# Performance work log

Hardware: AMD Instinct MI355X
Metric: run time of the kernel (lower is better)

## Reference

```python
import jax, jax.numpy as jnp
import numpy as np

B, L, C = 8, 512, 6        # graphs per batch, nodes per graph, atom channels
N = B * L
BOS = 0                    # global-node token id
ATOM_POS_PAD = 0           # atom position pad idx
BIGINT = 1e10

def setup_inputs() -> dict:
    key = jax.random.key(0)
    k1, k2, k3, k4 = jax.random.split(key, 4)
    X = jax.random.normal(k1, (N, C, 3), dtype=jnp.float32) * 5.0
    AP = jax.random.randint(k2, (N, C), 0, 8)              # 0 == atom_pos pad
    S = jax.random.randint(k3, (N,), 1, 16)
    S = S.at[jnp.arange(B) * L].set(BOS)                    # first node of each graph is BOS/global
    sec_pos = jax.random.randint(k4, (N,), 0, 4)
    batch_id = jnp.repeat(jnp.arange(B), L)
    return {"X": X, "AP": AP, "S": S, "sec_pos": sec_pos, "batch_id": batch_id, "k": 9}

def _knn_dist(X, AP, S):
    # per-graph pairwise node distance = min over atom-channel pairs of ||x_ic - x_jd||
    Xb = X.reshape(B, L, C, 3)
    sq = jnp.sum(Xb * Xb, axis=-1)                               # [B,L,C]
    dots = jnp.einsum('bicx,bjdx->bijcd', Xb, Xb)                # [B,L,L,C,C]
    d2 = sq[:, :, None, :, None] + sq[:, None, :, None, :] - 2.0 * dots
    dist = jnp.sqrt(jnp.maximum(d2, 0.0))
    pad = (AP.reshape(B, L, C) == ATOM_POS_PAD)
    pair_pad = pad[:, :, None, :, None] | pad[:, None, :, None, :]
    dist = dist + pair_pad.astype(dist.dtype) * BIGINT
    dist = jnp.min(dist.reshape(B, L, L, C * C), axis=-1)       # [B,L,L]
    # kNN only over non-global (not BOS) endpoints
    glb = (S.reshape(B, L) == BOS)
    gmask = glb[:, :, None] | glb[:, None, :]
    return jnp.where(gmask, jnp.asarray(BIGINT, dist.dtype), dist)

def reference(X, AP, S, sec_pos, batch_id, k):
    dist = _knn_dist(X, AP, S)
    neg_d, dst_local = jax.lax.top_k(-dist, k)                   # smallest-k per row, [B,L,k]
    dknn = (-neg_d).reshape(N, k)
    offs = jnp.arange(B) * L                                      # per-graph node offsets
    dst = (dst_local + offs[:, None, None]).reshape(N, k)
    src = jnp.broadcast_to(jnp.arange(N)[:, None], (N, k))
    valid = dknn < BIGINT
    valid = valid & (sec_pos[src] == sec_pos[dst])               # sec_pos[row]==sec_pos[col] filter
    dst = jnp.where(valid, dst, -1)                              # invalid edges marked -1 (static shape)
    # global edges: (0,j) for all j plus (i,0) for i>=1, per graph
    g_src_l = jnp.concatenate([jnp.zeros(L, jnp.int32), jnp.arange(1, L)])
    g_dst_l = jnp.concatenate([jnp.arange(L), jnp.zeros(L - 1, jnp.int32)])
    glb_edges = jnp.stack([
        (g_src_l[None, :] + offs[:, None]).reshape(-1),
        (g_dst_l[None, :] + offs[:, None]).reshape(-1)])
    # sequential edges among non-global nodes: |i-j|==1, i,j>=1
    a = jnp.arange(1, L - 1)
    s_src_l = jnp.concatenate([a, a + 1])
    s_dst_l = jnp.concatenate([a + 1, a])
    seq_edges = jnp.stack([
        (s_src_l[None, :] + offs[:, None]).reshape(-1),
        (s_dst_l[None, :] + offs[:, None]).reshape(-1)])
    return dknn, src, dst, valid, glb_edges, seq_edges
```

## Files before the change

### kernel.cpp

```cpp
#include <hip/hip_runtime.h>

#define B_  8
#define L_  512
#define C_  6
#define N_  (B_ * L_)
#define K_  9
#define BIGF 1e10f

#define NK        (N_ * K_)
#define OFF_DKNN  0
#define OFF_SRC   (NK)
#define OFF_DST   (2 * NK)
#define OFF_VALID (3 * NK)
#define OFF_GLB   (4 * NK)
#define GLB_PER   (2 * L_ - 1)
#define GLB_TOT   (2 * B_ * GLB_PER)
#define OFF_SEQ   (OFF_GLB + GLB_TOT)
#define SEQ_PER   (2 * (L_ - 2))
#define SEQ_TOT   (2 * B_ * SEQ_PER)

#define TPB 512
#define RPB 8

#define XFLOATS (L_ * C_ * 3)
#define X4      (XFLOATS / 4)
#define AP4     (L_ * C_ / 4)

static __device__ __forceinline__ unsigned umin32(unsigned a, unsigned b) {
    return a < b ? a : b;
}

__global__ __launch_bounds__(TPB, 4) void fused_kernel(const float* __restrict__ X,
                                                       const int* __restrict__ AP,
                                                       const int* __restrict__ S,
                                                       const int* __restrict__ sec,
                                                       float* __restrict__ out) {
    __shared__ float4 ch[C_][L_];
    __shared__ int sbuf[L_];

    const int tid = threadIdx.x;
    const int lane = tid & 63;
    const int wv = tid >> 6;
    const int row = blockIdx.x * RPB + wv;
    const int base = row & ~(L_ - 1);
    const int rl = row & (L_ - 1);

    float* lds = (float*)&ch[0][0];

    {
        const float4* Xs = (const float4*)(X + (size_t)base * (C_ * 3));
        float4* L4 = (float4*)lds;
#pragma unroll
        for (int i = 0; i < 5; ++i) {
            const int idx = tid + i * TPB;
            if (idx < X4) L4[idx] = Xs[idx];
        }
        const int4* As = (const int4*)(AP + (size_t)base * C_);
        int4* LA = (int4*)(lds + XFLOATS);
#pragma unroll
        for (int i = 0; i < 2; ++i) {
            const int idx = tid + i * TPB;
            if (idx < AP4) LA[idx] = As[idx];
        }
        sbuf[tid] = S[base + tid];
    }

    {
        const int gt = blockIdx.x * TPB + tid;
        if (gt < GLB_TOT) {
            const int r = gt / (B_ * GLB_PER);
            const int rem = gt % (B_ * GLB_PER);
            const int b = rem / GLB_PER;
            const int q = rem % GLB_PER;
            int v;
            if (r == 0) v = (q < L_) ? 0 : (q - (L_ - 1));
            else        v = (q < L_) ? q : 0;
            out[OFF_GLB + gt] = (float)(v + b * L_);
        }
        if (gt < SEQ_TOT) {
            const int r = gt / (B_ * SEQ_PER);
            const int rem = gt % (B_ * SEQ_PER);
            const int b = rem / SEQ_PER;
            const int q = rem % SEQ_PER;
            int v;
            if (r == 0) v = (q < L_ - 2) ? (q + 1) : (q - (L_ - 2) + 2);
            else        v = (q < L_ - 2) ? (q + 2) : (q - (L_ - 2) + 1);
            out[OFF_SEQ + gt] = (float)(v + b * L_);
        }
    }

    __syncthreads();

    float4 rrec[C_];
    {
        float xr[18];
        const float2* me = (const float2*)(lds + tid * 18);
#pragma unroll
        for (int j = 0; j < 9; ++j) {
            const float2 t = me[j];
            xr[2 * j] = t.x; xr[2 * j + 1] = t.y;
        }
        const int* apme = ((const int*)(lds + XFLOATS)) + tid * C_;
        int apv[C_];
#pragma unroll
        for (int c = 0; c < C_; ++c) apv[c] = apme[c];
        const float bias_g = (sbuf[tid] == 0) ? BIGF : 0.0f;
#pragma unroll
        for (int c = 0; c < C_; ++c) {
            const float a = xr[3 * c], b = xr[3 * c + 1], d = xr[3 * c + 2];
            float sq = (a * a + b * b) + d * d + bias_g;
            if (apv[c] == 0) sq += BIGF;
            rrec[c] = make_float4(a, b, d, sq);
        }
    }
    __syncthreads();

#pragma unroll
    for (int c = 0; c < C_; ++c) ch[c][tid] = rrec[c];
    __syncthreads();

    float ax[C_], ay[C_], az[C_], sc[C_];
#pragma unroll
    for (int c = 0; c < C_; ++c) {
        const float4 q = ch[c][rl];
        ax[c] = -2.0f * q.x; ay[c] = -2.0f * q.y; az[c] = -2.0f * q.z;
        sc[c] = q.w;
    }

    unsigned v[8];
#pragma unroll
    for (int s = 0; s < 8; ++s) {
        const int col = s * 64 + lane;
        float m = 3.0e38f;
#pragma unroll
        for (int d = 0; d < C_; ++d) {
            const float4 q = ch[d][col];
            const float t0 = fmaf(az[0], q.z, fmaf(ay[0], q.y, fmaf(ax[0], q.x, sc[0])));
            const float t1 = fmaf(az[1], q.z, fmaf(ay[1], q.y, fmaf(ax[1], q.x, sc[1])));
            const float t2 = fmaf(az[2], q.z, fmaf(ay[2], q.y, fmaf(ax[2], q.x, sc[2])));
            const float t3 = fmaf(az[3], q.z, fmaf(ay[3], q.y, fmaf(ax[3], q.x, sc[3])));
            const float t4 = fmaf(az[4], q.z, fmaf(ay[4], q.y, fmaf(ax[4], q.x, sc[4])));
            const float t5 = fmaf(az[5], q.z, fmaf(ay[5], q.y, fmaf(ax[5], q.x, sc[5])));
            const float m012 = fminf(fminf(t0, t1), t2);
            const float m345 = fminf(fminf(t3, t4), t5);
            m = fminf(m, fminf(m012, m345) + q.w);
        }
        m = fmaxf(m, 0.0f);
        v[s] = (__float_as_uint(m) & 0xFFFFFE00u) | (unsigned)col;
    }

    unsigned mine = 0xFFFFFFFFu;
#pragma unroll
    for (int t = 0; t < K_; ++t) {
        unsigned loc = v[0];
#pragma unroll
        for (int s = 1; s < 8; ++s) loc = umin32(loc, v[s]);
#pragma unroll
        for (int off = 32; off >= 1; off >>= 1) {
            const unsigned o = (unsigned)__shfl_xor((int)loc, off, 64);
            loc = umin32(loc, o);
        }
        if (lane == t) mine = loc;
#pragma unroll
        for (int s = 0; s < 8; ++s)
            v[s] = (v[s] == loc) ? 0xFFFFFFFFu : v[s];
    }

    if (lane < K_) {
        const int col = (int)(mine & 511u);
        const float d2 = __uint_as_float(mine & 0xFFFFFE00u);
        const bool masked = (d2 >= 1.0e9f);
        const float dval = masked ? BIGF : sqrtf(d2);
        const int dst = base + col;
        const bool valid = !masked && (sec[row] == sec[dst]);
        const size_t o = (size_t)row * K_ + lane;
        out[OFF_DKNN + o]  = dval;
        out[OFF_SRC + o]   = (float)row;
        out[OFF_DST + o]   = valid ? (float)dst : -1.0f;
        out[OFF_VALID + o] = valid ? 1.0f : 0.0f;
    }
}

extern "C" void kernel_launch(void* const* d_in, const int* in_sizes, int n_in,
                              void* d_out, int out_size, void* d_ws, size_t ws_size,
                              hipStream_t stream) {
    (void)in_sizes; (void)n_in; (void)out_size; (void)d_ws; (void)ws_size;
    const float* X   = (const float*)d_in[0];
    const int*   AP  = (const int*)d_in[1];
    const int*   S   = (const int*)d_in[2];
    const int*   sec = (const int*)d_in[3];
    float* out = (float*)d_out;

    hipLaunchKernelGGL(fused_kernel, dim3(N_ / RPB), dim3(TPB), 0, stream,
                       X, AP, S, sec, out);
}
```

Measured before the change: 75.50 us.

## Split each row's column scan across two waves and merge top-k candidates

Each query row is now handled by two waves, each scanning half of the 512 columns and producing its own local top-9. The two candidate lists are then merged through shared memory into a final top-9 by one wave. Rows per block drop from 8 to 4, so the grid doubles, and the launch-bounds occupancy hint rises from 4 to 6. This shortens each wave's serial distance and selection loop and adds parallelism, at the cost of loading the whole graph into LDS twice as often, an extra block barrier, and a second selection pass.

Result: slower. 79.81 us (+5.7%).

```diff
diff --git a/kernel.cpp b/kernel.cpp
--- a/kernel.cpp
+++ b/kernel.cpp
@@ -20,7 +20,8 @@
 #define SEQ_TOT   (2 * B_ * SEQ_PER)
 
 #define TPB 512
-#define RPB 8
+#define RPB 4
+#define HALF_COLS 256
 
 #define XFLOATS (L_ * C_ * 3)
 #define X4      (XFLOATS / 4)
@@ -30,18 +31,21 @@
     return a < b ? a : b;
 }
 
-__global__ __launch_bounds__(TPB, 4) void fused_kernel(const float* __restrict__ X,
+__global__ __launch_bounds__(TPB, 6) void fused_kernel(const float* __restrict__ X,
                                                        const int* __restrict__ AP,
                                                        const int* __restrict__ S,
                                                        const int* __restrict__ sec,
                                                        float* __restrict__ out) {
     __shared__ float4 ch[C_][L_];
     __shared__ int sbuf[L_];
+    __shared__ unsigned cand[RPB][32];
 
     const int tid = threadIdx.x;
     const int lane = tid & 63;
     const int wv = tid >> 6;
-    const int row = blockIdx.x * RPB + wv;
+    const int r = wv >> 1;
+    const int h = wv & 1;
+    const int row = blockIdx.x * RPB + r;
     const int base = row & ~(L_ - 1);
     const int rl = row & (L_ - 1);
 
@@ -68,23 +72,23 @@
     {
         const int gt = blockIdx.x * TPB + tid;
         if (gt < GLB_TOT) {
-            const int r = gt / (B_ * GLB_PER);
+            const int rr = gt / (B_ * GLB_PER);
             const int rem = gt % (B_ * GLB_PER);
             const int b = rem / GLB_PER;
             const int q = rem % GLB_PER;
             int v;
-            if (r == 0) v = (q < L_) ? 0 : (q - (L_ - 1));
-            else        v = (q < L_) ? q : 0;
+            if (rr == 0) v = (q < L_) ? 0 : (q - (L_ - 1));
+            else         v = (q < L_) ? q : 0;
             out[OFF_GLB + gt] = (float)(v + b * L_);
         }
         if (gt < SEQ_TOT) {
-            const int r = gt / (B_ * SEQ_PER);
+            const int rr = gt / (B_ * SEQ_PER);
             const int rem = gt % (B_ * SEQ_PER);
             const int b = rem / SEQ_PER;
             const int q = rem % SEQ_PER;
             int v;
-            if (r == 0) v = (q < L_ - 2) ? (q + 1) : (q - (L_ - 2) + 2);
-            else        v = (q < L_ - 2) ? (q + 2) : (q - (L_ - 2) + 1);
+            if (rr == 0) v = (q < L_ - 2) ? (q + 1) : (q - (L_ - 2) + 2);
+            else         v = (q < L_ - 2) ? (q + 2) : (q - (L_ - 2) + 1);
             out[OFF_SEQ + gt] = (float)(v + b * L_);
         }
     }
@@ -93,23 +97,14 @@
 
     float4 rrec[C_];
     {
-        float xr[18];
-        const float2* me = (const float2*)(lds + tid * 18);
-#pragma unroll
-        for (int j = 0; j < 9; ++j) {
-            const float2 t = me[j];
-            xr[2 * j] = t.x; xr[2 * j + 1] = t.y;
-        }
+        const float* meF = lds + tid * 18;
         const int* apme = ((const int*)(lds + XFLOATS)) + tid * C_;
-        int apv[C_];
-#pragma unroll
-        for (int c = 0; c < C_; ++c) apv[c] = apme[c];
         const float bias_g = (sbuf[tid] == 0) ? BIGF : 0.0f;
 #pragma unroll
         for (int c = 0; c < C_; ++c) {
-            const float a = xr[3 * c], b = xr[3 * c + 1], d = xr[3 * c + 2];
+            const float a = meF[3 * c], b = meF[3 * c + 1], d = meF[3 * c + 2];
             float sq = (a * a + b * b) + d * d + bias_g;
-            if (apv[c] == 0) sq += BIGF;
+            if (apme[c] == 0) sq += BIGF;
             rrec[c] = make_float4(a, b, d, sq);
         }
     }
@@ -127,10 +122,10 @@
         sc[c] = q.w;
     }
 
-    unsigned v[8];
-#pragma unroll
-    for (int s = 0; s < 8; ++s) {
-        const int col = s * 64 + lane;
+    unsigned v[4];
+#pragma unroll
+    for (int s = 0; s < 4; ++s) {
+        const int col = (h << 8) + (s << 6) + lane;
         float m = 3.0e38f;
 #pragma unroll
         for (int d = 0; d < C_; ++d) {
@@ -152,9 +147,7 @@
     unsigned mine = 0xFFFFFFFFu;
 #pragma unroll
     for (int t = 0; t < K_; ++t) {
-        unsigned loc = v[0];
-#pragma unroll
-        for (int s = 1; s < 8; ++s) loc = umin32(loc, v[s]);
+        unsigned loc = umin32(umin32(v[0], v[1]), umin32(v[2], v[3]));
 #pragma unroll
         for (int off = 32; off >= 1; off >>= 1) {
             const unsigned o = (unsigned)__shfl_xor((int)loc, off, 64);
@@ -162,22 +155,41 @@
         }
         if (lane == t) mine = loc;
 #pragma unroll
-        for (int s = 0; s < 8; ++s)
+        for (int s = 0; s < 4; ++s)
             v[s] = (v[s] == loc) ? 0xFFFFFFFFu : v[s];
     }
 
-    if (lane < K_) {
-        const int col = (int)(mine & 511u);
-        const float d2 = __uint_as_float(mine & 0xFFFFFE00u);
-        const bool masked = (d2 >= 1.0e9f);
-        const float dval = masked ? BIGF : sqrtf(d2);
-        const int dst = base + col;
-        const bool valid = !masked && (sec[row] == sec[dst]);
-        const size_t o = (size_t)row * K_ + lane;
-        out[OFF_DKNN + o]  = dval;
-        out[OFF_SRC + o]   = (float)row;
-        out[OFF_DST + o]   = valid ? (float)dst : -1.0f;
-        out[OFF_VALID + o] = valid ? 1.0f : 0.0f;
+    if (lane < 16) cand[r][(h << 4) + lane] = mine;
+    __syncthreads();
+
+    if (h == 0) {
+        unsigned cv = (lane < 32) ? cand[r][lane] : 0xFFFFFFFFu;
+        unsigned fin = 0xFFFFFFFFu;
+#pragma unroll
+        for (int t = 0; t < K_; ++t) {
+            unsigned loc = cv;
+#pragma unroll
+            for (int off = 16; off >= 1; off >>= 1) {
+                const unsigned o = (unsigned)__shfl_xor((int)loc, off, 64);
+                loc = umin32(loc, o);
+            }
+            if (lane == t) fin = loc;
+            cv = (cv == loc) ? 0xFFFFFFFFu : cv;
+        }
+
+        if (lane < K_) {
+            const int col = (int)(fin & 511u);
+            const float d2 = __uint_as_float(fin & 0xFFFFFE00u);
+            const bool masked = (d2 >= 1.0e9f);
+            const float dval = masked ? BIGF : sqrtf(d2);
+            const int dst = base + col;
+            const bool valid = !masked && (sec[row] == sec[dst]);
+            const size_t o = (size_t)row * K_ + lane;
+            out[OFF_DKNN + o]  = dval;
+            out[OFF_SRC + o]   = (float)row;
+            out[OFF_DST + o]   = valid ? (float)dst : -1.0f;
+            out[OFF_VALID + o] = valid ? 1.0f : 0.0f;
+        }
     }
 }
 
```
